# Kernel optimization log

Hardware: AMD Instinct MI355X
Metric: run time of the kernel (lower is better)

Reference implementation:

```python
import jax, jax.numpy as jnp
import numpy as np
import math

B, L, D_IN = 4, 8192, 64
H = 256          # d_model
N2 = 32          # d_state // 2 complex conjugate pairs (S4D)
NL = 4           # n_layers
D_OUT = 10


def setup_inputs() -> dict:
    key = jax.random.key(0)
    ks = jax.random.split(key, 16)
    x = jax.random.normal(ks[0], (B, L, D_IN), dtype=jnp.float32)
    # encoder Linear(d_input, d_model)
    enc_W = jax.random.normal(ks[1], (H, D_IN), dtype=jnp.float32) / np.sqrt(D_IN)
    enc_b = jnp.zeros((H,), dtype=jnp.float32)
    # per-layer S4D parameters (stacked over n_layers)
    log_dt = jax.random.uniform(ks[2], (NL, H), dtype=jnp.float32,
                                minval=math.log(1e-3), maxval=math.log(1e-1))
    log_A_re = jnp.full((NL, H, N2), math.log(0.5), dtype=jnp.float32)
    A_im = jnp.tile(math.pi * jnp.arange(N2, dtype=jnp.float32), (NL, H, 1))
    C_re = jax.random.normal(ks[3], (NL, H, N2), dtype=jnp.float32) * (0.5 ** 0.5)
    C_im = jax.random.normal(ks[4], (NL, H, N2), dtype=jnp.float32) * (0.5 ** 0.5)
    D = jax.random.normal(ks[5], (NL, H), dtype=jnp.float32)
    # S4 block output linear (H -> 2H) followed by GLU
    Wo = jax.random.normal(ks[6], (NL, 2 * H, H), dtype=jnp.float32) / np.sqrt(H)
    bo = jnp.zeros((NL, 2 * H), dtype=jnp.float32)
    # post-norm LayerNorm over d_model
    ln_w = jnp.ones((NL, H), dtype=jnp.float32)
    ln_b = jnp.zeros((NL, H), dtype=jnp.float32)
    # final decoder Linear(d_model, d_output)
    out_W = jax.random.normal(ks[7], (D_OUT, H), dtype=jnp.float32) / np.sqrt(H)
    out_b = jnp.zeros((D_OUT,), dtype=jnp.float32)
    return dict(x=x, enc_W=enc_W, enc_b=enc_b, log_dt=log_dt, log_A_re=log_A_re,
                A_im=A_im, C_re=C_re, C_im=C_im, D=D, Wo=Wo, bo=bo,
                ln_w=ln_w, ln_b=ln_b, out_W=out_W, out_b=out_b)


def _s4d_kernel(log_dt, log_A_re, A_im, C_re, C_im, L):
    # S4D-ZOH-ish (S4D-Lin) kernel: K[h,l] = 2 Re sum_n C~[h,n] exp(l*dt*A[h,n])
    dt = jnp.exp(log_dt)[:, None]                      # (H,1)
    A = -jnp.exp(log_A_re) + 1j * A_im                 # (H,N2)
    dtA = dt * A                                       # (H,N2)
    Ct = (C_re + 1j * C_im) * (jnp.exp(dtA) - 1.0) / A # (H,N2)
    t = jnp.arange(L, dtype=jnp.float32)
    V = jnp.exp(dtA[:, :, None] * t)                   # (H,N2,L) Vandermonde
    return 2.0 * jnp.einsum('hn,hnl->hl', Ct, V).real  # (H,L)


def reference(x, enc_W, enc_b, log_dt, log_A_re, A_im, C_re, C_im, D, Wo, bo,
              ln_w, ln_b, out_W, out_b):
    Bc, Lc, _ = x.shape
    h = x @ enc_W.T + enc_b          # (B,L,H)
    h = h.transpose(0, 2, 1)         # (B,H,L) (transposed layout)
    n_layers = log_dt.shape[0]
    for i in range(n_layers):
        K = _s4d_kernel(log_dt[i], log_A_re[i], A_im[i], C_re[i], C_im[i], Lc)
        # FFT convolution (causal, non-circular via 2L padding)
        Kf = jnp.fft.rfft(K, n=2 * Lc)                       # (H, L+1)
        hf = jnp.fft.rfft(h, n=2 * Lc)                       # (B,H,L+1)
        y = jnp.fft.irfft(hf * Kf, n=2 * Lc)[..., :Lc]
        y = y + D[i][:, None] * h                            # skip D*u
        y = jax.nn.gelu(y)
        # output linear (H -> 2H) + GLU, pointwise over length
        u = jnp.einsum('oh,bhl->bol', Wo[i], y) + bo[i][:, None]
        Hd = h.shape[1]
        z = u[:, :Hd] * jax.nn.sigmoid(u[:, Hd:])
        h = z + h                                            # residual
        # post-norm LayerNorm over channel (d_model) dim
        mu = h.mean(axis=1, keepdims=True)
        var = h.var(axis=1, keepdims=True)
        h = (h - mu) / jnp.sqrt(var + 1e-5) * ln_w[i][:, None] + ln_b[i][:, None]
    h = h.transpose(0, 2, 1)          # (B,L,H)
    return h @ out_W.T + out_b        # (B,L,d_output)
```

## Files before the change

### kernel.cpp

```cpp
#include <hip/hip_runtime.h>
#include <hip/hip_bf16.h>


constexpr int B_ = 4, L_ = 8192, DIN = 64, H_ = 256, N2_ = 32, NL_ = 4, DOUT = 10;
constexpr int LC = 64, CHK = L_ / LC;
constexpr int GCH = B_ * CHK;
constexpr int M_ = B_ * L_;

constexpr size_t OFF_XB   = 0;
constexpr size_t OFF_EWB  = 1048576;
constexpr size_t OFF_WOB  = 8388608;
constexpr size_t OFF_PW   = 8650752;
constexpr size_t OFF_PCT  = 8716288;
constexpr size_t OFF_PWLC = 8781824;
constexpr size_t OFF_PZ   = 8847360;
constexpr size_t OFF_UCM  = 8929280;
constexpr size_t OFF_YCM  = 13123584;
constexpr size_t OFF_MTA  = 17317888;
constexpr size_t OFF_MWA  = 19415040;
constexpr size_t OFF_MVA  = 21512192;

typedef short bf16x8 __attribute__((ext_vector_type(8)));
typedef short short8 __attribute__((ext_vector_type(8)));
typedef float f32x4  __attribute__((ext_vector_type(4)));
typedef int   int2v  __attribute__((ext_vector_type(2)));

__device__ __forceinline__ float b2f(short s) {
    union { float f; unsigned u; } c;
    c.u = ((unsigned)(unsigned short)s) << 16;
    return c.f;
}

__global__ __launch_bounds__(256) void k_params(
    const float* __restrict__ log_dt, const float* __restrict__ log_A_re,
    const float* __restrict__ A_im, const float* __restrict__ C_re,
    const float* __restrict__ C_im, float* __restrict__ ws)
{
    int idx = blockIdx.x * 256 + threadIdx.x;
    if (idx >= NL_ * H_ * N2_) return;
    int i  = idx / (H_ * N2_);
    int hh = (idx / N2_) % H_;
    float dt  = expf(log_dt[i * H_ + hh]);
    float Are = -expf(log_A_re[idx]);
    float Aim = A_im[idx];
    float zre = dt * Are, zim = dt * Aim;
    float er  = expf(zre);
    float wre = er * cosf(zim), wim = er * sinf(zim);
    float d   = Are * Are + Aim * Aim;
    float nre = wre - 1.f, nim = wim;
    float qre = (nre * Are + nim * Aim) / d;
    float qim = (nim * Are - nre * Aim) / d;
    float cr = C_re[idx], ci = C_im[idx];
    float ctre = cr * qre - ci * qim;
    float ctim = cr * qim + ci * qre;
    float er2 = expf(zre * (float)LC);
    float wlre = er2 * cosf(zim * (float)LC);
    float wlim = er2 * sinf(zim * (float)LC);
    ((float2*)(ws + OFF_PW))[idx]   = make_float2(wre, wim);
    ((float2*)(ws + OFF_PCT))[idx]  = make_float2(2.f * ctre, 2.f * ctim);
    ((float2*)(ws + OFF_PWLC))[idx] = make_float2(wlre, wlim);
    ((float2*)(ws + OFF_PZ))[idx]   = make_float2(zre, zim);
}

__global__ __launch_bounds__(256) void k_mats_all(const float* __restrict__ ws,
    __hip_bfloat16* __restrict__ mt, __hip_bfloat16* __restrict__ mw,
    __hip_bfloat16* __restrict__ mv)
{
    int bid = blockIdx.x;
    int layer = bid >> 8, h = bid & 255;
    int lh = layer * H_ + h;
    int tid = threadIdx.x;
    __shared__ float zre[32], zim[32], ctr[32], cti[32], kv[64];
    if (tid < 32) {
        float2 z = ((const float2*)(ws + OFF_PZ))[(size_t)lh * N2_ + tid];
        float2 c = ((const float2*)(ws + OFF_PCT))[(size_t)lh * N2_ + tid];
        zre[tid] = z.x; zim[tid] = z.y; ctr[tid] = c.x; cti[tid] = c.y;
    }
    __syncthreads();
    if (tid < 64) {
        float d = (float)tid, acc = 0.f;
        for (int n = 0; n < 32; n++) {
            float er = expf(zre[n] * d);
            float co = cosf(zim[n] * d), si = sinf(zim[n] * d);
            acc += er * (ctr[n] * co - cti[n] * si);
        }
        kv[tid] = acc;
    }
    __syncthreads();
    {
        int t = tid >> 2, j0 = (tid & 3) * 16;
        alignas(16) __hip_bfloat16 row[16];
        #pragma unroll
        for (int jj = 0; jj < 16; jj++) {
            int j = j0 + jj;
            row[jj] = __float2bfloat16(j <= t ? kv[t - j] : 0.f);
        }
        *(short8*)(mt + (size_t)lh*4096 + t*64 + j0)     = *(short8*)&row[0];
        *(short8*)(mt + (size_t)lh*4096 + t*64 + j0 + 8) = *(short8*)&row[8];
    }
    {
        int n = tid >> 3, j0 = (tid & 7) * 8;
        alignas(16) __hip_bfloat16 rre[8], rim[8];
        #pragma unroll
        for (int jj = 0; jj < 8; jj++) {
            float e = (float)(63 - (j0 + jj));
            float er = expf(zre[n] * e);
            rre[jj] = __float2bfloat16(er * cosf(zim[n] * e));
            rim[jj] = __float2bfloat16(er * sinf(zim[n] * e));
        }
        *(short8*)(mw + (size_t)lh*4096 + (2*n)*64 + j0)   = *(short8*)&rre[0];
        *(short8*)(mw + (size_t)lh*4096 + (2*n+1)*64 + j0) = *(short8*)&rim[0];
    }
    {
        int t = tid >> 2, n0 = (tid & 3) * 8;
        float e = (float)(t + 1);
        alignas(16) __hip_bfloat16 row[16];
        #pragma unroll
        for (int k = 0; k < 8; k++) {
            int n = n0 + k;
            float er = expf(zre[n] * e);
            float wr = er * cosf(zim[n] * e), wi = er * sinf(zim[n] * e);
            row[2*k]   = __float2bfloat16(ctr[n]*wr - cti[n]*wi);
            row[2*k+1] = __float2bfloat16(-(ctr[n]*wi + cti[n]*wr));
        }
        *(short8*)(mv + (size_t)lh*4096 + t*64 + 2*n0)     = *(short8*)&row[0];
        *(short8*)(mv + (size_t)lh*4096 + t*64 + 2*n0 + 8) = *(short8*)&row[8];
    }
}

__global__ __launch_bounds__(256) void k_wcvt(const float* __restrict__ src,
    __hip_bfloat16* __restrict__ dst, int n4)
{
    int i = blockIdx.x * 256 + threadIdx.x;
    if (i >= n4) return;
    float4 v = ((const float4*)src)[i];
    union { __hip_bfloat16 b[4]; uint2 u; } o;
    o.b[0] = __float2bfloat16(v.x); o.b[1] = __float2bfloat16(v.y);
    o.b[2] = __float2bfloat16(v.z); o.b[3] = __float2bfloat16(v.w);
    ((uint2*)dst)[i] = o.u;
}

__global__ __launch_bounds__(256) void k_encoder(const __hip_bfloat16* __restrict__ xb,
    const __hip_bfloat16* __restrict__ ewb, const float* __restrict__ enc_b,
    __hip_bfloat16* __restrict__ u)
{
    __shared__ short lt[256 * 66];
    int tid = threadIdx.x;
    int w = tid >> 6, l = tid & 63, l15 = l & 15, l4 = l >> 4;
    int m0 = blockIdx.x * 64;
    int nv = w * 64;
    f32x4 acc[4][4];
    #pragma unroll
    for (int mi = 0; mi < 4; mi++)
        #pragma unroll
        for (int nj = 0; nj < 4; nj++) acc[mi][nj] = (f32x4)0.f;
    #pragma unroll
    for (int ks = 0; ks < 2; ks++) {
        int k0 = ks * 32 + l4 * 8;
        bf16x8 a[4];
        #pragma unroll
        for (int mi = 0; mi < 4; mi++)
            a[mi] = *(const bf16x8*)(xb + (size_t)(m0 + mi * 16 + l15) * 64 + k0);
        #pragma unroll
        for (int nj = 0; nj < 4; nj++) {
            bf16x8 b = *(const bf16x8*)(ewb + (size_t)(nv + nj * 16 + l15) * 64 + k0);
            #pragma unroll
            for (int mi = 0; mi < 4; mi++)
                acc[mi][nj] = __builtin_amdgcn_mfma_f32_16x16x32_bf16(a[mi], b, acc[mi][nj], 0, 0, 0);
        }
    }
    float bov[4];
    #pragma unroll
    for (int nj = 0; nj < 4; nj++) bov[nj] = enc_b[nv + nj * 16 + l15];
    #pragma unroll
    for (int mi = 0; mi < 4; mi++)
        #pragma unroll
        for (int r = 0; r < 4; r++) {
            int lr = mi * 16 + l4 * 4 + r;
            #pragma unroll
            for (int nj = 0; nj < 4; nj++) {
                int cn = nv + nj * 16 + l15;
                __hip_bfloat16 bv = __float2bfloat16(acc[mi][nj][r] + bov[nj]);
                lt[cn * 66 + lr] = *(short*)&bv;
            }
        }
    __syncthreads();
    #pragma unroll
    for (int q = 0; q < 8; q++)
        *(short8*)(u + (size_t)tid * M_ + m0 + q * 8) = *(short8*)&lt[tid * 66 + q * 8];
}

__global__ __launch_bounds__(256) void k_ssm(const __hip_bfloat16* __restrict__ ucm,
    const __hip_bfloat16* __restrict__ mt, const __hip_bfloat16* __restrict__ mw,
    const __hip_bfloat16* __restrict__ mv, const float* __restrict__ ws, int layer,
    const float* __restrict__ Dp, __hip_bfloat16* __restrict__ ycm)
{
    __shared__ __hip_bfloat16 ulds[L_];
    __shared__ __hip_bfloat16 st[CHK * 64];
    __shared__ float segT[8][32][2];
    int h = blockIdx.x >> 2, b = blockIdx.x & 3;
    int tid = threadIdx.x, w = tid >> 6, l = tid & 63, l15 = l & 15, l4 = l >> 4;
    const __hip_bfloat16* ub = ucm + (size_t)h * M_ + (size_t)b * L_;
    #pragma unroll
    for (int it = 0; it < 4; it++) {
        int e0 = it * 2048 + tid * 8;
        short8 v = *(const short8*)(ub + e0);
        int c = e0 >> 6, e = e0 & 63;
        *(short8*)&ulds[c * 64 + (e ^ ((c & 7) << 3))] = v;
    }
    __syncthreads();
    {
        const __hip_bfloat16* bbase = mw + (size_t)h * 4096 + l15 * 64 + l4 * 8;
        #pragma unroll
        for (int half = 0; half < 2; half++) {
            int g0 = (w + half * 4) * 16;
            int ca = g0 + l15;
            f32x4 acc[4];
            #pragma unroll
            for (int nj = 0; nj < 4; nj++) acc[nj] = (f32x4)0.f;
            #pragma unroll
            for (int ks = 0; ks < 2; ks++) {
                int e = l4 * 8 + ks * 32;
                bf16x8 a = *(const bf16x8*)&ulds[ca * 64 + (e ^ ((ca & 7) << 3))];
                #pragma unroll
                for (int nj = 0; nj < 4; nj++) {
                    bf16x8 bb = *(const bf16x8*)(bbase + nj * 16 * 64 + ks * 32);
                    acc[nj] = __builtin_amdgcn_mfma_f32_16x16x32_bf16(a, bb, acc[nj], 0, 0, 0);
                }
            }
            #pragma unroll
            for (int nj = 0; nj < 4; nj++)
                #pragma unroll
                for (int r = 0; r < 4; r++) {
                    int c = g0 + l4 * 4 + r, e = nj * 16 + l15;
                    st[c * 64 + (e ^ ((c & 7) << 3))] = __float2bfloat16(acc[nj][r]);
                }
        }
    }
    __syncthreads();
    {
        int s = tid >> 5, n = tid & 31;
        float2 wl = ((const float2*)(ws + OFF_PWLC))[(size_t)layer * H_ * N2_ + h * 32 + n];
        float tr = 0.f, ti = 0.f;
        for (int j = 0; j < 16; j++) {
            int c = s * 16 + j;
            __hip_bfloat162* p = (__hip_bfloat162*)&st[c * 64 + ((2 * n) ^ ((c & 7) << 3))];
            float2 v = __bfloat1622float2(*p);
            float nr = fmaf(wl.x, tr, v.x); nr = fmaf(-wl.y, ti, nr);
            float ni = fmaf(wl.x, ti, v.y); ni = fmaf(wl.y, tr, ni);
            tr = nr; ti = ni;
        }
        segT[s][n][0] = tr; segT[s][n][1] = ti;
        __syncthreads();
        float wr = wl.x, wi = wl.y;
        #pragma unroll
        for (int q = 0; q < 4; q++) {
            float nr = wr * wr - wi * wi, ni = 2.f * wr * wi;
            wr = nr; wi = ni;
        }
        float ar = 0.f, ai = 0.f;
        for (int t = 0; t < s; t++) {
            float Tx = segT[t][n][0], Ty = segT[t][n][1];
            float nr = fmaf(wr, ar, Tx); nr = fmaf(-wi, ai, nr);
            float ni = fmaf(wr, ai, Ty); ni = fmaf(wi, ar, ni);
            ar = nr; ai = ni;
        }
        for (int j = 0; j < 16; j++) {
            int c = s * 16 + j;
            __hip_bfloat162* p = (__hip_bfloat162*)&st[c * 64 + ((2 * n) ^ ((c & 7) << 3))];
            float2 v = __bfloat1622float2(*p);
            *p = __float22bfloat162_rn(make_float2(ar, ai));
            float nr = fmaf(wl.x, ar, v.x); nr = fmaf(-wl.y, ai, nr);
            float ni = fmaf(wl.x, ai, v.y); ni = fmaf(wl.y, ar, ni);
            ar = nr; ai = ni;
        }
    }
    __syncthreads();
    {
        const __hip_bfloat16* bt = mt + (size_t)h * 4096 + l15 * 64 + l4 * 8;
        const __hip_bfloat16* bv = mv + (size_t)h * 4096 + l15 * 64 + l4 * 8;
        float Dh = Dp[layer * H_ + h];
        __hip_bfloat16* yb = ycm + (size_t)h * M_ + (size_t)b * L_;
        #pragma unroll
        for (int half = 0; half < 2; half++) {
            int g0 = (w + half * 4) * 16;
            int ca = g0 + l15;
            f32x4 acc[4];
            #pragma unroll
            for (int nj = 0; nj < 4; nj++) acc[nj] = (f32x4)0.f;
            #pragma unroll
            for (int ks = 0; ks < 2; ks++) {
                int e = l4 * 8 + ks * 32;
                bf16x8 a = *(const bf16x8*)&ulds[ca * 64 + (e ^ ((ca & 7) << 3))];
                #pragma unroll
                for (int nj = 0; nj < 4; nj++) {
                    bf16x8 bb = *(const bf16x8*)(bt + nj * 16 * 64 + ks * 32);
                    acc[nj] = __builtin_amdgcn_mfma_f32_16x16x32_bf16(a, bb, acc[nj], 0, 0, 0);
                }
            }
            #pragma unroll
            for (int ks = 0; ks < 2; ks++) {
                int e = l4 * 8 + ks * 32;
                bf16x8 a = *(const bf16x8*)&st[ca * 64 + (e ^ ((ca & 7) << 3))];
                #pragma unroll
                for (int nj = 0; nj < 4; nj++) {
                    bf16x8 bb = *(const bf16x8*)(bv + nj * 16 * 64 + ks * 32);
                    acc[nj] = __builtin_amdgcn_mfma_f32_16x16x32_bf16(a, bb, acc[nj], 0, 0, 0);
                }
            }
            #pragma unroll
            for (int nj = 0; nj < 4; nj++)
                #pragma unroll
                for (int r = 0; r < 4; r++) {
                    int g = g0 + l4 * 4 + r;
                    int e = nj * 16 + l15;
                    float uv = __bfloat162float(ulds[g * 64 + (e ^ ((g & 7) << 3))]);
                    float v = fmaf(Dh, uv, acc[nj][r]);
                    float gg = 0.7978845608028654f * fmaf(0.044715f * v, v * v, v);
                    float yv = v / (1.f + __expf(-2.f * gg));
                    yb[(size_t)g * 64 + nj * 16 + l15] = __float2bfloat16(yv);
                }
        }
    }
}

__global__ __launch_bounds__(256) void k_glu_mfma(
    const __hip_bfloat16* __restrict__ ycm,
    const __hip_bfloat16* __restrict__ wob,
    const float* __restrict__ bo, const float* __restrict__ lnw,
    const float* __restrict__ lnb,
    __hip_bfloat16* __restrict__ u)
{
    __shared__ int buf[8320];
    __shared__ float red[4][32][2];
    int* bufA = buf;
    int* bufR = buf + 4160;
    int tid = threadIdx.x;
    int w = tid >> 6, l = tid & 63, l15 = l & 15, l4 = l >> 4;
    int mb = blockIdx.x * 64;
    int nv = w * 64;
    int p = tid & 127, ph = tid >> 7;
    const __hip_bfloat16* aB = ycm + (size_t)(2 * p) * M_ + mb + ph * 16;
    const __hip_bfloat16* rB = u + (size_t)(2 * p) * M_ + mb + ph * 16;

    short8 A0[4], R0[4], A1[4], R1[4];
    A0[0] = *(const short8*)(aB);          A0[1] = *(const short8*)(aB + 8);
    A0[2] = *(const short8*)(aB + M_);     A0[3] = *(const short8*)(aB + M_ + 8);
    R0[0] = *(const short8*)(rB);          R0[1] = *(const short8*)(rB + 8);
    R0[2] = *(const short8*)(rB + M_);     R0[3] = *(const short8*)(rB + M_ + 8);
    A1[0] = *(const short8*)(aB + 32);     A1[1] = *(const short8*)(aB + 40);
    A1[2] = *(const short8*)(aB + M_ + 32);A1[3] = *(const short8*)(aB + M_ + 40);

    float bov[4], bog[4], lw[4], lb[4];
    #pragma unroll
    for (int nj = 0; nj < 4; nj++) {
        int cn = nv + nj * 16 + l15;
        bov[nj] = bo[cn]; bog[nj] = bo[256 + cn];
        lw[nj] = lnw[cn]; lb[nj] = lnb[cn];
    }

    {
        int* da = bufA + ph * 16 * 130 + p;
        int* dr = bufR + ph * 16 * 130 + p;
        #pragma unroll
        for (int j = 0; j < 8; j++) {
            da[j * 130]       = ((int)(unsigned short)A0[0][j]) | (((int)(unsigned short)A0[2][j]) << 16);
            da[(8 + j) * 130] = ((int)(unsigned short)A0[1][j]) | (((int)(unsigned short)A0[3][j]) << 16);
            dr[j * 130]       = ((int)(unsigned short)R0[0][j]) | (((int)(unsigned short)R0[2][j]) << 16);
            dr[(8 + j) * 130] = ((int)(unsigned short)R0[1][j]) | (((int)(unsigned short)R0[3][j]) << 16);
        }
    }
    __syncthreads();

    int abase0 = l15 * 130 + l4 * 4;
    #pragma unroll
    for (int tile = 0; tile < 2; tile++) {
        int m0 = mb + tile * 32;
        f32x4 accv[2][4], accg[2][4];
        #pragma unroll
        for (int sub = 0; sub < 2; sub++)
            #pragma unroll
            for (int nj = 0; nj < 4; nj++) { accv[sub][nj] = (f32x4)0.f; accg[sub][nj] = (f32x4)0.f; }

        #pragma unroll 2
        for (int ks = 0; ks < 8; ks++) {
            int k0 = ks * 32 + l4 * 8;
            union { int2v d[2]; bf16x8 v; } a0u, a1u;
            a0u.d[0] = *(const int2v*)&bufA[abase0 + ks * 16];
            a0u.d[1] = *(const int2v*)&bufA[abase0 + ks * 16 + 2];
            a1u.d[0] = *(const int2v*)&bufA[abase0 + 16 * 130 + ks * 16];
            a1u.d[1] = *(const int2v*)&bufA[abase0 + 16 * 130 + ks * 16 + 2];
            bf16x8 a0 = a0u.v;
            bf16x8 a1 = a1u.v;
            #pragma unroll
            for (int nj = 0; nj < 4; nj++) {
                bf16x8 bv = *(const bf16x8*)(wob + (size_t)(nv + nj * 16 + l15) * H_ + k0);
                bf16x8 bg = *(const bf16x8*)(wob + (size_t)(256 + nv + nj * 16 + l15) * H_ + k0);
                accv[0][nj] = __builtin_amdgcn_mfma_f32_16x16x32_bf16(a0, bv, accv[0][nj], 0, 0, 0);
                accg[0][nj] = __builtin_amdgcn_mfma_f32_16x16x32_bf16(a0, bg, accg[0][nj], 0, 0, 0);
                accv[1][nj] = __builtin_amdgcn_mfma_f32_16x16x32_bf16(a1, bv, accv[1][nj], 0, 0, 0);
                accg[1][nj] = __builtin_amdgcn_mfma_f32_16x16x32_bf16(a1, bg, accg[1][nj], 0, 0, 0);
            }
        }

        const short* bufRs = (const short*)bufR;
        #pragma unroll
        for (int sub = 0; sub < 2; sub++) {
            #pragma unroll
            for (int r = 0; r < 4; r++) {
                int lr = sub * 16 + l4 * 4 + r;
                float s = 0.f, ss = 0.f;
                #pragma unroll
                for (int nj = 0; nj < 4; nj++) {
                    int cn = nv + nj * 16 + l15;
                    float uv = accv[sub][nj][r] + bov[nj];
                    float ug = accg[sub][nj][r] + bog[nj];
                    float z = uv / (1.f + __expf(-ug));
                    float v = z + b2f(bufRs[lr * 260 + cn]);
                    accv[sub][nj][r] = v;
                    s += v; ss += v * v;
                }
                #pragma unroll
                for (int off = 1; off < 16; off <<= 1) {
                    s  += __shfl_xor(s, off);
                    ss += __shfl_xor(ss, off);
                }
                if (l15 == 0) { red[w][lr][0] = s; red[w][lr][1] = ss; }
            }
        }
        if (tile == 0) {
            R1[0] = *(const short8*)(rB + 32);      R1[1] = *(const short8*)(rB + 40);
            R1[2] = *(const short8*)(rB + M_ + 32); R1[3] = *(const short8*)(rB + M_ + 40);
        }
        __syncthreads();
        short* lt = (short*)buf;
        #pragma unroll
        for (int sub = 0; sub < 2; sub++) {
            #pragma unroll
            for (int r = 0; r < 4; r++) {
                int lr = sub * 16 + l4 * 4 + r;
                float s  = red[0][lr][0] + red[1][lr][0] + red[2][lr][0] + red[3][lr][0];
                float ss = red[0][lr][1] + red[1][lr][1] + red[2][lr][1] + red[3][lr][1];
                float mu = s * (1.f / 256.f);
                float var = ss * (1.f / 256.f) - mu * mu;
                float rstd = rsqrtf(var + 1e-5f);
                #pragma unroll
                for (int nj = 0; nj < 4; nj++) {
                    int cn = nv + nj * 16 + l15;
                    float val = (accv[sub][nj][r] - mu) * rstd * lw[nj] + lb[nj];
                    __hip_bfloat16 bval = __float2bfloat16(val);
                    lt[cn * 34 + lr] = *(short*)&bval;
                }
            }
        }
        __syncthreads();
        #pragma unroll
        for (int q = 0; q < 4; q++)
            *(short8*)(u + (size_t)tid * M_ + m0 + q * 8)
                = *(short8*)&lt[tid * 34 + q * 8];
        if (tile == 0) {
            __syncthreads();
            int* da = bufA + ph * 16 * 130 + p;
            int* dr = bufR + ph * 16 * 130 + p;
            #pragma unroll
            for (int j = 0; j < 8; j++) {
                da[j * 130]       = ((int)(unsigned short)A1[0][j]) | (((int)(unsigned short)A1[2][j]) << 16);
                da[(8 + j) * 130] = ((int)(unsigned short)A1[1][j]) | (((int)(unsigned short)A1[3][j]) << 16);
                dr[j * 130]       = ((int)(unsigned short)R1[0][j]) | (((int)(unsigned short)R1[2][j]) << 16);
                dr[(8 + j) * 130] = ((int)(unsigned short)R1[1][j]) | (((int)(unsigned short)R1[3][j]) << 16);
            }
            __syncthreads();
        }
    }
}

__global__ __launch_bounds__(256) void k_decoder(const __hip_bfloat16* __restrict__ u,
    const float* __restrict__ out_W, const float* __restrict__ out_b,
    float* __restrict__ out)
{
    __shared__ int ds[64 * 130];
    __shared__ float wl[10][260];
    int m0 = blockIdx.x * 64;
    int tid = threadIdx.x;
    {
        int p = tid & 127, ph = tid >> 7;
        const __hip_bfloat16* s0 = u + (size_t)(2 * p) * M_ + m0 + ph * 32;
        const __hip_bfloat16* s1 = s0 + M_;
        short8 y0[4], y1[4];
        #pragma unroll
        for (int q = 0; q < 4; q++) {
            y0[q] = *(const short8*)(s0 + q * 8);
            y1[q] = *(const short8*)(s1 + q * 8);
        }
        int* dst = ds + (ph * 32) * 130 + p;
        #pragma unroll
        for (int q = 0; q < 4; q++)
            #pragma unroll
            for (int j = 0; j < 8; j++)
                dst[(q * 8 + j) * 130] =
                    ((int)(unsigned short)y0[q][j]) | (((int)(unsigned short)y1[q][j]) << 16);
    }
    for (int q = tid; q < 640; q += 256) {
        int r = q / 64, k4 = q % 64;
        *(float4*)&wl[r][k4 * 4] = ((const float4*)out_W)[q];
    }
    __syncthreads();
    int slot = tid & 15;
    if (slot < DOUT) {
        #pragma unroll
        for (int pass = 0; pass < 4; pass++) {
            int pl = pass * 16 + (tid >> 4);
            const int* row = ds + pl * 130;
            float a0 = 0.f, a1 = 0.f;
            #pragma unroll 8
            for (int d = 0; d < 128; d++) {
                int v = row[d];
                a0 = fmaf(b2f((short)(v & 0xffff)),  wl[slot][2 * d],     a0);
                a1 = fmaf(b2f((short)(v >> 16)),     wl[slot][2 * d + 1], a1);
            }
            out[(size_t)(m0 + pl) * DOUT + slot] = a0 + a1 + out_b[slot];
        }
    }
}

extern "C" void kernel_launch(void* const* d_in, const int* in_sizes, int n_in,
                              void* d_out, int out_size, void* d_ws, size_t ws_size,
                              hipStream_t stream)
{
    (void)in_sizes; (void)n_in; (void)out_size; (void)ws_size;
    const float* x        = (const float*)d_in[0];
    const float* enc_W    = (const float*)d_in[1];
    const float* enc_b    = (const float*)d_in[2];
    const float* log_dt   = (const float*)d_in[3];
    const float* log_A_re = (const float*)d_in[4];
    const float* A_im     = (const float*)d_in[5];
    const float* C_re     = (const float*)d_in[6];
    const float* C_im     = (const float*)d_in[7];
    const float* Dp       = (const float*)d_in[8];
    const float* Wo       = (const float*)d_in[9];
    const float* bo       = (const float*)d_in[10];
    const float* lnw      = (const float*)d_in[11];
    const float* lnb      = (const float*)d_in[12];
    const float* out_W    = (const float*)d_in[13];
    const float* out_b    = (const float*)d_in[14];
    float* ws = (float*)d_ws;
    __hip_bfloat16* xb  = (__hip_bfloat16*)(ws + OFF_XB);
    __hip_bfloat16* ewb = (__hip_bfloat16*)(ws + OFF_EWB);
    __hip_bfloat16* u   = (__hip_bfloat16*)(ws + OFF_UCM);
    __hip_bfloat16* ycm = (__hip_bfloat16*)(ws + OFF_YCM);
    __hip_bfloat16* mtA = (__hip_bfloat16*)(ws + OFF_MTA);
    __hip_bfloat16* mwA = (__hip_bfloat16*)(ws + OFF_MWA);
    __hip_bfloat16* mvA = (__hip_bfloat16*)(ws + OFF_MVA);
    __hip_bfloat16* wob = (__hip_bfloat16*)(ws + OFF_WOB);

    k_params<<<NL_ * H_ * N2_ / 256, 256, 0, stream>>>(log_dt, log_A_re, A_im, C_re, C_im, ws);
    k_wcvt<<<(NL_ * 2 * H_ * H_ / 4 + 255) / 256, 256, 0, stream>>>(Wo, wob, NL_ * 2 * H_ * H_ / 4);
    k_wcvt<<<(M_ * DIN / 4 + 255) / 256, 256, 0, stream>>>(x, xb, M_ * DIN / 4);
    k_wcvt<<<(H_ * DIN / 4 + 255) / 256, 256, 0, stream>>>(enc_W, ewb, H_ * DIN / 4);
    k_mats_all<<<NL_ * H_, 256, 0, stream>>>(ws, mtA, mwA, mvA);
    k_encoder<<<M_ / 64, 256, 0, stream>>>(xb, ewb, enc_b, u);
    for (int i = 0; i < NL_; i++) {
        k_ssm<<<H_ * B_, 256, 0, stream>>>(u,
            mtA + (size_t)i * H_ * 4096, mwA + (size_t)i * H_ * 4096,
            mvA + (size_t)i * H_ * 4096, ws, i, Dp, ycm);
        k_glu_mfma<<<M_ / 64, 256, 0, stream>>>(ycm,
            wob + (size_t)i * 2 * H_ * H_, bo + (size_t)i * 2 * H_,
            lnw + (size_t)i * H_, lnb + (size_t)i * H_, u);
    }
    k_decoder<<<M_ / 64, 256, 0, stream>>>(u, out_W, out_b, (float*)d_out);
}
```

Measured before the change: 366.5 us.

## Fuse param setup, x conversion, and decoder into neighboring kernels

```diff
diff --git a/kernel.cpp b/kernel.cpp
--- a/kernel.cpp
+++ b/kernel.cpp
@@ -4,16 +4,11 @@
 
 constexpr int B_ = 4, L_ = 8192, DIN = 64, H_ = 256, N2_ = 32, NL_ = 4, DOUT = 10;
 constexpr int LC = 64, CHK = L_ / LC;
-constexpr int GCH = B_ * CHK;
 constexpr int M_ = B_ * L_;
 
-constexpr size_t OFF_XB   = 0;
 constexpr size_t OFF_EWB  = 1048576;
 constexpr size_t OFF_WOB  = 8388608;
-constexpr size_t OFF_PW   = 8650752;
-constexpr size_t OFF_PCT  = 8716288;
 constexpr size_t OFF_PWLC = 8781824;
-constexpr size_t OFF_PZ   = 8847360;
 constexpr size_t OFF_UCM  = 8929280;
 constexpr size_t OFF_YCM  = 13123584;
 constexpr size_t OFF_MTA  = 17317888;
@@ -22,6 +17,7 @@
 
 typedef short bf16x8 __attribute__((ext_vector_type(8)));
 typedef short short8 __attribute__((ext_vector_type(8)));
+typedef short short4v __attribute__((ext_vector_type(4)));
 typedef float f32x4  __attribute__((ext_vector_type(4)));
 typedef int   int2v  __attribute__((ext_vector_type(2)));
 
@@ -29,103 +25,6 @@
     union { float f; unsigned u; } c;
     c.u = ((unsigned)(unsigned short)s) << 16;
     return c.f;
-}
-
-__global__ __launch_bounds__(256) void k_params(
-    const float* __restrict__ log_dt, const float* __restrict__ log_A_re,
-    const float* __restrict__ A_im, const float* __restrict__ C_re,
-    const float* __restrict__ C_im, float* __restrict__ ws)
-{
-    int idx = blockIdx.x * 256 + threadIdx.x;
-    if (idx >= NL_ * H_ * N2_) return;
-    int i  = idx / (H_ * N2_);
-    int hh = (idx / N2_) % H_;
-    float dt  = expf(log_dt[i * H_ + hh]);
-    float Are = -expf(log_A_re[idx]);
-    float Aim = A_im[idx];
-    float zre = dt * Are, zim = dt * Aim;
-    float er  = expf(zre);
-    float wre = er * cosf(zim), wim = er * sinf(zim);
-    float d   = Are * Are + Aim * Aim;
-    float nre = wre - 1.f, nim = wim;
-    float qre = (nre * Are + nim * Aim) / d;
-    float qim = (nim * Are - nre * Aim) / d;
-    float cr = C_re[idx], ci = C_im[idx];
-    float ctre = cr * qre - ci * qim;
-    float ctim = cr * qim + ci * qre;
-    float er2 = expf(zre * (float)LC);
-    float wlre = er2 * cosf(zim * (float)LC);
-    float wlim = er2 * sinf(zim * (float)LC);
-    ((float2*)(ws + OFF_PW))[idx]   = make_float2(wre, wim);
-    ((float2*)(ws + OFF_PCT))[idx]  = make_float2(2.f * ctre, 2.f * ctim);
-    ((float2*)(ws + OFF_PWLC))[idx] = make_float2(wlre, wlim);
-    ((float2*)(ws + OFF_PZ))[idx]   = make_float2(zre, zim);
-}
-
-__global__ __launch_bounds__(256) void k_mats_all(const float* __restrict__ ws,
-    __hip_bfloat16* __restrict__ mt, __hip_bfloat16* __restrict__ mw,
-    __hip_bfloat16* __restrict__ mv)
-{
-    int bid = blockIdx.x;
-    int layer = bid >> 8, h = bid & 255;
-    int lh = layer * H_ + h;
-    int tid = threadIdx.x;
-    __shared__ float zre[32], zim[32], ctr[32], cti[32], kv[64];
-    if (tid < 32) {
-        float2 z = ((const float2*)(ws + OFF_PZ))[(size_t)lh * N2_ + tid];
-        float2 c = ((const float2*)(ws + OFF_PCT))[(size_t)lh * N2_ + tid];
-        zre[tid] = z.x; zim[tid] = z.y; ctr[tid] = c.x; cti[tid] = c.y;
-    }
-    __syncthreads();
-    if (tid < 64) {
-        float d = (float)tid, acc = 0.f;
-        for (int n = 0; n < 32; n++) {
-            float er = expf(zre[n] * d);
-            float co = cosf(zim[n] * d), si = sinf(zim[n] * d);
-            acc += er * (ctr[n] * co - cti[n] * si);
-        }
-        kv[tid] = acc;
-    }
-    __syncthreads();
-    {
-        int t = tid >> 2, j0 = (tid & 3) * 16;
-        alignas(16) __hip_bfloat16 row[16];
-        #pragma unroll
-        for (int jj = 0; jj < 16; jj++) {
-            int j = j0 + jj;
-            row[jj] = __float2bfloat16(j <= t ? kv[t - j] : 0.f);
-        }
-        *(short8*)(mt + (size_t)lh*4096 + t*64 + j0)     = *(short8*)&row[0];
-        *(short8*)(mt + (size_t)lh*4096 + t*64 + j0 + 8) = *(short8*)&row[8];
-    }
-    {
-        int n = tid >> 3, j0 = (tid & 7) * 8;
-        alignas(16) __hip_bfloat16 rre[8], rim[8];
-        #pragma unroll
-        for (int jj = 0; jj < 8; jj++) {
-            float e = (float)(63 - (j0 + jj));
-            float er = expf(zre[n] * e);
-            rre[jj] = __float2bfloat16(er * cosf(zim[n] * e));
-            rim[jj] = __float2bfloat16(er * sinf(zim[n] * e));
-        }
-        *(short8*)(mw + (size_t)lh*4096 + (2*n)*64 + j0)   = *(short8*)&rre[0];
-        *(short8*)(mw + (size_t)lh*4096 + (2*n+1)*64 + j0) = *(short8*)&rim[0];
-    }
-    {
-        int t = tid >> 2, n0 = (tid & 3) * 8;
-        float e = (float)(t + 1);
-        alignas(16) __hip_bfloat16 row[16];
-        #pragma unroll
-        for (int k = 0; k < 8; k++) {
-            int n = n0 + k;
-            float er = expf(zre[n] * e);
-            float wr = er * cosf(zim[n] * e), wi = er * sinf(zim[n] * e);
-            row[2*k]   = __float2bfloat16(ctr[n]*wr - cti[n]*wi);
-            row[2*k+1] = __float2bfloat16(-(ctr[n]*wi + cti[n]*wr));
-        }
-        *(short8*)(mv + (size_t)lh*4096 + t*64 + 2*n0)     = *(short8*)&row[0];
-        *(short8*)(mv + (size_t)lh*4096 + t*64 + 2*n0 + 8) = *(short8*)&row[8];
-    }
 }
 
 __global__ __launch_bounds__(256) void k_wcvt(const float* __restrict__ src,
@@ -140,15 +39,114 @@
     ((uint2*)dst)[i] = o.u;
 }
 
-__global__ __launch_bounds__(256) void k_encoder(const __hip_bfloat16* __restrict__ xb,
+__global__ __launch_bounds__(256) void k_mats_all(
+    const float* __restrict__ log_dt, const float* __restrict__ log_A_re,
+    const float* __restrict__ A_im, const float* __restrict__ C_re,
+    const float* __restrict__ C_im, float* __restrict__ ws,
+    __hip_bfloat16* __restrict__ mt, __hip_bfloat16* __restrict__ mw,
+    __hip_bfloat16* __restrict__ mv)
+{
+    int bid = blockIdx.x;
+    int layer = bid >> 8, h = bid & 255;
+    int lh = layer * H_ + h;
+    int tid = threadIdx.x;
+    __shared__ float zre[32], zim[32], ctr[32], cti[32], kv[64];
+    if (tid < 32) {
+        int idx = lh * N2_ + tid;
+        float dt  = expf(log_dt[lh]);
+        float Are = -expf(log_A_re[idx]);
+        float Aim = A_im[idx];
+        float zr = dt * Are, zi = dt * Aim;
+        float er = expf(zr);
+        float wre = er * cosf(zi), wim = er * sinf(zi);
+        float d = Are * Are + Aim * Aim;
+        float nre = wre - 1.f, nim = wim;
+        float qre = (nre * Are + nim * Aim) / d;
+        float qim = (nim * Are - nre * Aim) / d;
+        float cr = C_re[idx], ci = C_im[idx];
+        zre[tid] = zr; zim[tid] = zi;
+        ctr[tid] = 2.f * (cr * qre - ci * qim);
+        cti[tid] = 2.f * (cr * qim + ci * qre);
+        float er2 = expf(zr * (float)LC);
+        ((float2*)(ws + OFF_PWLC))[idx] =
+            make_float2(er2 * cosf(zi * (float)LC), er2 * sinf(zi * (float)LC));
+    }
+    __syncthreads();
+    if (tid < 64) {
+        float d = (float)tid, acc = 0.f;
+        for (int n = 0; n < 32; n++) {
+            float er = expf(zre[n] * d);
+            float co = cosf(zim[n] * d), si = sinf(zim[n] * d);
+            acc += er * (ctr[n] * co - cti[n] * si);
+        }
+        kv[tid] = acc;
+    }
+    __syncthreads();
+    {
+        int t = tid >> 2, j0 = (tid & 3) * 16;
+        alignas(16) __hip_bfloat16 row[16];
+        #pragma unroll
+        for (int jj = 0; jj < 16; jj++) {
+            int j = j0 + jj;
+            row[jj] = __float2bfloat16(j <= t ? kv[t - j] : 0.f);
+        }
+        *(short8*)(mt + (size_t)lh*4096 + t*64 + j0)     = *(short8*)&row[0];
+        *(short8*)(mt + (size_t)lh*4096 + t*64 + j0 + 8) = *(short8*)&row[8];
+    }
+    {
+        int n = tid >> 3, j0 = (tid & 7) * 8;
+        alignas(16) __hip_bfloat16 rre[8], rim[8];
+        #pragma unroll
+        for (int jj = 0; jj < 8; jj++) {
+            float e = (float)(63 - (j0 + jj));
+            float er = expf(zre[n] * e);
+            rre[jj] = __float2bfloat16(er * cosf(zim[n] * e));
+            rim[jj] = __float2bfloat16(er * sinf(zim[n] * e));
+        }
+        *(short8*)(mw + (size_t)lh*4096 + (2*n)*64 + j0)   = *(short8*)&rre[0];
+        *(short8*)(mw + (size_t)lh*4096 + (2*n+1)*64 + j0) = *(short8*)&rim[0];
+    }
+    {
+        int t = tid >> 2, n0 = (tid & 3) * 8;
+        float e = (float)(t + 1);
+        alignas(16) __hip_bfloat16 row[16];
+        #pragma unroll
+        for (int k = 0; k < 8; k++) {
+            int n = n0 + k;
+            float er = expf(zre[n] * e);
+            float wr = er * cosf(zim[n] * e), wi = er * sinf(zim[n] * e);
+            row[2*k]   = __float2bfloat16(ctr[n]*wr - cti[n]*wi);
+            row[2*k+1] = __float2bfloat16(-(ctr[n]*wi + cti[n]*wr));
+        }
+        *(short8*)(mv + (size_t)lh*4096 + t*64 + 2*n0)     = *(short8*)&row[0];
+        *(short8*)(mv + (size_t)lh*4096 + t*64 + 2*n0 + 8) = *(short8*)&row[8];
+    }
+}
+
+__global__ __launch_bounds__(256) void k_encoder(const float* __restrict__ x,
     const __hip_bfloat16* __restrict__ ewb, const float* __restrict__ enc_b,
     __hip_bfloat16* __restrict__ u)
 {
-    __shared__ short lt[256 * 66];
+    __shared__ short sbuf[256 * 66];
+    short* xls = sbuf;
     int tid = threadIdx.x;
     int w = tid >> 6, l = tid & 63, l15 = l & 15, l4 = l >> 4;
     int m0 = blockIdx.x * 64;
     int nv = w * 64;
+    {
+        const float4* x4 = (const float4*)x;
+        #pragma unroll
+        for (int q = 0; q < 4; q++) {
+            int f = tid * 4 + q;
+            float4 v = x4[(size_t)m0 * 16 + f];
+            int e = f * 4, row = e >> 6, col = e & 63;
+            alignas(8) __hip_bfloat16 t4[4] = {
+                __float2bfloat16(v.x), __float2bfloat16(v.y),
+                __float2bfloat16(v.z), __float2bfloat16(v.w) };
+            *(short4v*)&xls[row * 72 + col] = *(short4v*)t4;
+        }
+    }
+    __syncthreads();
     f32x4 acc[4][4];
     #pragma unroll
     for (int mi = 0; mi < 4; mi++)
@@ -160,7 +158,7 @@
         bf16x8 a[4];
         #pragma unroll
         for (int mi = 0; mi < 4; mi++)
-            a[mi] = *(const bf16x8*)(xb + (size_t)(m0 + mi * 16 + l15) * 64 + k0);
+            a[mi] = *(const bf16x8*)&xls[(mi * 16 + l15) * 72 + k0];
         #pragma unroll
         for (int nj = 0; nj < 4; nj++) {
             bf16x8 b = *(const bf16x8*)(ewb + (size_t)(nv + nj * 16 + l15) * 64 + k0);
@@ -172,6 +170,7 @@
     float bov[4];
     #pragma unroll
     for (int nj = 0; nj < 4; nj++) bov[nj] = enc_b[nv + nj * 16 + l15];
+    __syncthreads();
     #pragma unroll
     for (int mi = 0; mi < 4; mi++)
         #pragma unroll
@@ -181,13 +180,13 @@
             for (int nj = 0; nj < 4; nj++) {
                 int cn = nv + nj * 16 + l15;
                 __hip_bfloat16 bv = __float2bfloat16(acc[mi][nj][r] + bov[nj]);
-                lt[cn * 66 + lr] = *(short*)&bv;
+                sbuf[cn * 66 + lr] = *(short*)&bv;
             }
         }
     __syncthreads();
     #pragma unroll
     for (int q = 0; q < 8; q++)
-        *(short8*)(u + (size_t)tid * M_ + m0 + q * 8) = *(short8*)&lt[tid * 66 + q * 8];
+        *(short8*)(u + (size_t)tid * M_ + m0 + q * 8) = *(short8*)&sbuf[tid * 66 + q * 8];
 }
 
 __global__ __launch_bounds__(256) void k_ssm(const __hip_bfloat16* __restrict__ ucm,
@@ -324,203 +323,185 @@
     }
 }
 
+#define GLU_BODY(DECODE)                                                        \
+    __shared__ int buf[8320];                                                   \
+    __shared__ float red[4][32][2];                                             \
+    int* bufA = buf;                                                            \
+    int* bufR = buf + 4160;                                                     \
+    int tid = threadIdx.x;                                                      \
+    int w = tid >> 6, l = tid & 63, l15 = l & 15, l4 = l >> 4;                  \
+    int mb = blockIdx.x * 64;                                                   \
+    int nv = w * 64;                                                            \
+    int p = tid & 127, ph = tid >> 7;                                           \
+    const __hip_bfloat16* aB = ycm + (size_t)(2 * p) * M_ + mb + ph * 16;       \
+    const __hip_bfloat16* rB = u + (size_t)(2 * p) * M_ + mb + ph * 16;         \
+    short8 A0[4], R0[4], A1[4], R1[4];                                          \
+    A0[0] = *(const short8*)(aB);          A0[1] = *(const short8*)(aB + 8);    \
+    A0[2] = *(const short8*)(aB + M_);     A0[3] = *(const short8*)(aB + M_ + 8);\
+    R0[0] = *(const short8*)(rB);          R0[1] = *(const short8*)(rB + 8);    \
+    R0[2] = *(const short8*)(rB + M_);     R0[3] = *(const short8*)(rB + M_ + 8);\
+    A1[0] = *(const short8*)(aB + 32);     A1[1] = *(const short8*)(aB + 40);   \
+    A1[2] = *(const short8*)(aB + M_ + 32);A1[3] = *(const short8*)(aB + M_ + 40);\
+    float bov[4], bog[4], lw[4], lb[4];                                         \
+    _Pragma("unroll")                                                           \
+    for (int nj = 0; nj < 4; nj++) {                                            \
+        int cn = nv + nj * 16 + l15;                                            \
+        bov[nj] = bo[cn]; bog[nj] = bo[256 + cn];                               \
+        lw[nj] = lnw[cn]; lb[nj] = lnb[cn];                                     \
+    }                                                                           \
+    {                                                                           \
+        int* da = bufA + ph * 16 * 130 + p;                                     \
+        int* dr = bufR + ph * 16 * 130 + p;                                     \
+        _Pragma("unroll")                                                       \
+        for (int j = 0; j < 8; j++) {                                           \
+            da[j * 130]       = ((int)(unsigned short)A0[0][j]) | (((int)(unsigned short)A0[2][j]) << 16);\
+            da[(8 + j) * 130] = ((int)(unsigned short)A0[1][j]) | (((int)(unsigned short)A0[3][j]) << 16);\
+            dr[j * 130]       = ((int)(unsigned short)R0[0][j]) | (((int)(unsigned short)R0[2][j]) << 16);\
+            dr[(8 + j) * 130] = ((int)(unsigned short)R0[1][j]) | (((int)(unsigned short)R0[3][j]) << 16);\
+        }                                                                       \
+    }                                                                           \
+    __syncthreads();                                                            \
+    int abase0 = l15 * 130 + l4 * 4;                                            \
+    _Pragma("unroll")                                                           \
+    for (int tile = 0; tile < 2; tile++) {                                      \
+        int m0 = mb + tile * 32;                                                \
+        f32x4 accv[2][4], accg[2][4];                                           \
+        _Pragma("unroll")                                                       \
+        for (int sub = 0; sub < 2; sub++)                                       \
+            _Pragma("unroll")                                                   \
+            for (int nj = 0; nj < 4; nj++) { accv[sub][nj] = (f32x4)0.f; accg[sub][nj] = (f32x4)0.f; }\
+        _Pragma("unroll 2")                                                     \
+        for (int ks = 0; ks < 8; ks++) {                                        \
+            int k0 = ks * 32 + l4 * 8;                                          \
+            union { int2v d[2]; bf16x8 v; } a0u, a1u;                           \
+            a0u.d[0] = *(const int2v*)&bufA[abase0 + ks * 16];                  \
+            a0u.d[1] = *(const int2v*)&bufA[abase0 + ks * 16 + 2];              \
+            a1u.d[0] = *(const int2v*)&bufA[abase0 + 16 * 130 + ks * 16];       \
+            a1u.d[1] = *(const int2v*)&bufA[abase0 + 16 * 130 + ks * 16 + 2];   \
+            bf16x8 a0 = a0u.v;                                                  \
+            bf16x8 a1 = a1u.v;                                                  \
+            _Pragma("unroll")                                                   \
+            for (int nj = 0; nj < 4; nj++) {                                    \
+                bf16x8 bv = *(const bf16x8*)(wob + (size_t)(nv + nj * 16 + l15) * H_ + k0);\
+                bf16x8 bg = *(const bf16x8*)(wob + (size_t)(256 + nv + nj * 16 + l15) * H_ + k0);\
+                accv[0][nj] = __builtin_amdgcn_mfma_f32_16x16x32_bf16(a0, bv, accv[0][nj], 0, 0, 0);\
+                accg[0][nj] = __builtin_amdgcn_mfma_f32_16x16x32_bf16(a0, bg, accg[0][nj], 0, 0, 0);\
+                accv[1][nj] = __builtin_amdgcn_mfma_f32_16x16x32_bf16(a1, bv, accv[1][nj], 0, 0, 0);\
+                accg[1][nj] = __builtin_amdgcn_mfma_f32_16x16x32_bf16(a1, bg, accg[1][nj], 0, 0, 0);\
+            }                                                                   \
+        }                                                                       \
+        const short* bufRs = (const short*)bufR;                                \
+        _Pragma("unroll")                                                       \
+        for (int sub = 0; sub < 2; sub++) {                                     \
+            _Pragma("unroll")                                                   \
+            for (int r = 0; r < 4; r++) {                                       \
+                int lr = sub * 16 + l4 * 4 + r;                                 \
+                float s = 0.f, ss = 0.f;                                        \
+                _Pragma("unroll")                                               \
+                for (int nj = 0; nj < 4; nj++) {                                \
+                    int cn = nv + nj * 16 + l15;                                \
+                    float uv = accv[sub][nj][r] + bov[nj];                      \
+                    float ug = accg[sub][nj][r] + bog[nj];                      \
+                    float z = uv / (1.f + __expf(-ug));                         \
+                    float v = z + b2f(bufRs[lr * 260 + cn]);                    \
+                    accv[sub][nj][r] = v;                                       \
+                    s += v; ss += v * v;                                        \
+                }                                                               \
+                _Pragma("unroll")                                               \
+                for (int off = 1; off < 16; off <<= 1) {                        \
+                    s  += __shfl_xor(s, off);                                   \
+                    ss += __shfl_xor(ss, off);                                  \
+                }                                                               \
+                if (l15 == 0) { red[w][lr][0] = s; red[w][lr][1] = ss; }        \
+            }                                                                   \
+        }                                                                       \
+        if (tile == 0) {                                                        \
+            R1[0] = *(const short8*)(rB + 32);      R1[1] = *(const short8*)(rB + 40);\
+            R1[2] = *(const short8*)(rB + M_ + 32); R1[3] = *(const short8*)(rB + M_ + 40);\
+        }                                                                       \
+        __syncthreads();                                                        \
+        short* lt = (short*)buf;                                                \
+        _Pragma("unroll")                                                       \
+        for (int sub = 0; sub < 2; sub++) {                                     \
+            _Pragma("unroll")                                                   \
+            for (int r = 0; r < 4; r++) {                                       \
+                int lr = sub * 16 + l4 * 4 + r;                                 \
+                float s  = red[0][lr][0] + red[1][lr][0] + red[2][lr][0] + red[3][lr][0];\
+                float ss = red[0][lr][1] + red[1][lr][1] + red[2][lr][1] + red[3][lr][1];\
+                float mu = s * (1.f / 256.f);                                   \
+                float var = ss * (1.f / 256.f) - mu * mu;                       \
+                float rstd = rsqrtf(var + 1e-5f);                               \
+                _Pragma("unroll")                                               \
+                for (int nj = 0; nj < 4; nj++) {                                \
+                    int cn = nv + nj * 16 + l15;                                \
+                    float val = (accv[sub][nj][r] - mu) * rstd * lw[nj] + lb[nj];\
+                    __hip_bfloat16 bval = __float2bfloat16(val);                \
+                    lt[cn * 34 + lr] = *(short*)&bval;                          \
+                }                                                               \
+            }                                                                   \
+        }                                                                       \
+        __syncthreads();                                                        \
+        _Pragma("unroll")                                                       \
+        for (int q = 0; q < 4; q++)                                             \
+            *(short8*)(u + (size_t)tid * M_ + m0 + q * 8)                       \
+                = *(short8*)&lt[tid * 34 + q * 8];                              \
+        if (DECODE) {                                                           \
+            float* wl2 = (float*)(buf + 4608);                                  \
+            for (int q = tid; q < 2560; q += 256) {                             \
+                int row = q >> 8, col = q & 255;                                \
+                wl2[row * 257 + col] = out_W[q];                                \
+            }                                                                   \
+            __syncthreads();                                                    \
+            int slot = tid & 15, pbase = tid >> 4;                              \
+            if (slot < DOUT) {                                                  \
+                _Pragma("unroll")                                               \
+                for (int pass = 0; pass < 2; pass++) {                          \
+                    int lr = pass * 16 + pbase;                                 \
+                    const short* ltp = lt + lr;                                 \
+                    const float* wp = wl2 + slot * 257;                         \
+                    float a0 = 0.f, a1 = 0.f;                                   \
+                    _Pragma("unroll 8")                                         \
+                    for (int cn = 0; cn < 256; cn += 2) {                       \
+                        a0 = fmaf(b2f(ltp[cn * 34]),       wp[cn],     a0);     \
+                        a1 = fmaf(b2f(ltp[(cn + 1) * 34]), wp[cn + 1], a1);     \
+                    }                                                           \
+                    out[(size_t)(m0 + lr) * DOUT + slot] = a0 + a1 + out_b[slot];\
+                }                                                               \
+            }                                                                   \
+        }                                                                       \
+        if (tile == 0) {                                                        \
+            __syncthreads();                                                    \
+            int* da = bufA + ph * 16 * 130 + p;                                 \
+            int* dr = bufR + ph * 16 * 130 + p;                                 \
+            _Pragma("unroll")                                                   \
+            for (int j = 0; j < 8; j++) {                                       \
+                da[j * 130]       = ((int)(unsigned short)A1[0][j]) | (((int)(unsigned short)A1[2][j]) << 16);\
+                da[(8 + j) * 130] = ((int)(unsigned short)A1[1][j]) | (((int)(unsigned short)A1[3][j]) << 16);\
+                dr[j * 130]       = ((int)(unsigned short)R1[0][j]) | (((int)(unsigned short)R1[2][j]) << 16);\
+                dr[(8 + j) * 130] = ((int)(unsigned short)R1[1][j]) | (((int)(unsigned short)R1[3][j]) << 16);\
+            }                                                                   \
+            __syncthreads();                                                    \
+        }                                                                       \
+    }
+
 __global__ __launch_bounds__(256) void k_glu_mfma(
-    const __hip_bfloat16* __restrict__ ycm,
-    const __hip_bfloat16* __restrict__ wob,
+    const __hip_bfloat16* __restrict__ ycm, const __hip_bfloat16* __restrict__ wob,
     const float* __restrict__ bo, const float* __restrict__ lnw,
-    const float* __restrict__ lnb,
-    __hip_bfloat16* __restrict__ u)
-{
-    __shared__ int buf[8320];
-    __shared__ float red[4][32][2];
-    int* bufA = buf;
-    int* bufR = buf + 4160;
-    int tid = threadIdx.x;
-    int w = tid >> 6, l = tid & 63, l15 = l & 15, l4 = l >> 4;
-    int mb = blockIdx.x * 64;
-    int nv = w * 64;
-    int p = tid & 127, ph = tid >> 7;
-    const __hip_bfloat16* aB = ycm + (size_t)(2 * p) * M_ + mb + ph * 16;
-    const __hip_bfloat16* rB = u + (size_t)(2 * p) * M_ + mb + ph * 16;
-
-    short8 A0[4], R0[4], A1[4], R1[4];
-    A0[0] = *(const short8*)(aB);          A0[1] = *(const short8*)(aB + 8);
-    A0[2] = *(const short8*)(aB + M_);     A0[3] = *(const short8*)(aB + M_ + 8);
-    R0[0] = *(const short8*)(rB);          R0[1] = *(const short8*)(rB + 8);
-    R0[2] = *(const short8*)(rB + M_);     R0[3] = *(const short8*)(rB + M_ + 8);
-    A1[0] = *(const short8*)(aB + 32);     A1[1] = *(const short8*)(aB + 40);
-    A1[2] = *(const short8*)(aB + M_ + 32);A1[3] = *(const short8*)(aB + M_ + 40);
-
-    float bov[4], bog[4], lw[4], lb[4];
-    #pragma unroll
-    for (int nj = 0; nj < 4; nj++) {
-        int cn = nv + nj * 16 + l15;
-        bov[nj] = bo[cn]; bog[nj] = bo[256 + cn];
-        lw[nj] = lnw[cn]; lb[nj] = lnb[cn];
-    }
-
-    {
-        int* da = bufA + ph * 16 * 130 + p;
-        int* dr = bufR + ph * 16 * 130 + p;
-        #pragma unroll
-        for (int j = 0; j < 8; j++) {
-            da[j * 130]       = ((int)(unsigned short)A0[0][j]) | (((int)(unsigned short)A0[2][j]) << 16);
-            da[(8 + j) * 130] = ((int)(unsigned short)A0[1][j]) | (((int)(unsigned short)A0[3][j]) << 16);
-            dr[j * 130]       = ((int)(unsigned short)R0[0][j]) | (((int)(unsigned short)R0[2][j]) << 16);
-            dr[(8 + j) * 130] = ((int)(unsigned short)R0[1][j]) | (((int)(unsigned short)R0[3][j]) << 16);
-        }
-    }
-    __syncthreads();
-
-    int abase0 = l15 * 130 + l4 * 4;
-    #pragma unroll
-    for (int tile = 0; tile < 2; tile++) {
-        int m0 = mb + tile * 32;
-        f32x4 accv[2][4], accg[2][4];
-        #pragma unroll
-        for (int sub = 0; sub < 2; sub++)
-            #pragma unroll
-            for (int nj = 0; nj < 4; nj++) { accv[sub][nj] = (f32x4)0.f; accg[sub][nj] = (f32x4)0.f; }
-
-        #pragma unroll 2
-        for (int ks = 0; ks < 8; ks++) {
-            int k0 = ks * 32 + l4 * 8;
-            union { int2v d[2]; bf16x8 v; } a0u, a1u;
-            a0u.d[0] = *(const int2v*)&bufA[abase0 + ks * 16];
-            a0u.d[1] = *(const int2v*)&bufA[abase0 + ks * 16 + 2];
-            a1u.d[0] = *(const int2v*)&bufA[abase0 + 16 * 130 + ks * 16];
-            a1u.d[1] = *(const int2v*)&bufA[abase0 + 16 * 130 + ks * 16 + 2];
-            bf16x8 a0 = a0u.v;
-            bf16x8 a1 = a1u.v;
-            #pragma unroll
-            for (int nj = 0; nj < 4; nj++) {
-                bf16x8 bv = *(const bf16x8*)(wob + (size_t)(nv + nj * 16 + l15) * H_ + k0);
-                bf16x8 bg = *(const bf16x8*)(wob + (size_t)(256 + nv + nj * 16 + l15) * H_ + k0);
-                accv[0][nj] = __builtin_amdgcn_mfma_f32_16x16x32_bf16(a0, bv, accv[0][nj], 0, 0, 0);
-                accg[0][nj] = __builtin_amdgcn_mfma_f32_16x16x32_bf16(a0, bg, accg[0][nj], 0, 0, 0);
-                accv[1][nj] = __builtin_amdgcn_mfma_f32_16x16x32_bf16(a1, bv, accv[1][nj], 0, 0, 0);
-                accg[1][nj] = __builtin_amdgcn_mfma_f32_16x16x32_bf16(a1, bg, accg[1][nj], 0, 0, 0);
-            }
-        }
-
-        const short* bufRs = (const short*)bufR;
-        #pragma unroll
-        for (int sub = 0; sub < 2; sub++) {
-            #pragma unroll
-            for (int r = 0; r < 4; r++) {
-                int lr = sub * 16 + l4 * 4 + r;
-                float s = 0.f, ss = 0.f;
-                #pragma unroll
-                for (int nj = 0; nj < 4; nj++) {
-                    int cn = nv + nj * 16 + l15;
-                    float uv = accv[sub][nj][r] + bov[nj];
-                    float ug = accg[sub][nj][r] + bog[nj];
-                    float z = uv / (1.f + __expf(-ug));
-                    float v = z + b2f(bufRs[lr * 260 + cn]);
-                    accv[sub][nj][r] = v;
-                    s += v; ss += v * v;
-                }
-                #pragma unroll
-                for (int off = 1; off < 16; off <<= 1) {
-                    s  += __shfl_xor(s, off);
-                    ss += __shfl_xor(ss, off);
-                }
-                if (l15 == 0) { red[w][lr][0] = s; red[w][lr][1] = ss; }
-            }
-        }
-        if (tile == 0) {
-            R1[0] = *(const short8*)(rB + 32);      R1[1] = *(const short8*)(rB + 40);
-            R1[2] = *(const short8*)(rB + M_ + 32); R1[3] = *(const short8*)(rB + M_ + 40);
-        }
-        __syncthreads();
-        short* lt = (short*)buf;
-        #pragma unroll
-        for (int sub = 0; sub < 2; sub++) {
-            #pragma unroll
-            for (int r = 0; r < 4; r++) {
-                int lr = sub * 16 + l4 * 4 + r;
-                float s  = red[0][lr][0] + red[1][lr][0] + red[2][lr][0] + red[3][lr][0];
-                float ss = red[0][lr][1] + red[1][lr][1] + red[2][lr][1] + red[3][lr][1];
-                float mu = s * (1.f / 256.f);
-                float var = ss * (1.f / 256.f) - mu * mu;
-                float rstd = rsqrtf(var + 1e-5f);
-                #pragma unroll
-                for (int nj = 0; nj < 4; nj++) {
-                    int cn = nv + nj * 16 + l15;
-                    float val = (accv[sub][nj][r] - mu) * rstd * lw[nj] + lb[nj];
-                    __hip_bfloat16 bval = __float2bfloat16(val);
-                    lt[cn * 34 + lr] = *(short*)&bval;
-                }
-            }
-        }
-        __syncthreads();
-        #pragma unroll
-        for (int q = 0; q < 4; q++)
-            *(short8*)(u + (size_t)tid * M_ + m0 + q * 8)
-                = *(short8*)&lt[tid * 34 + q * 8];
-        if (tile == 0) {
-            __syncthreads();
-            int* da = bufA + ph * 16 * 130 + p;
-            int* dr = bufR + ph * 16 * 130 + p;
-            #pragma unroll
-            for (int j = 0; j < 8; j++) {
-                da[j * 130]       = ((int)(unsigned short)A1[0][j]) | (((int)(unsigned short)A1[2][j]) << 16);
-                da[(8 + j) * 130] = ((int)(unsigned short)A1[1][j]) | (((int)(unsigned short)A1[3][j]) << 16);
-                dr[j * 130]       = ((int)(unsigned short)R1[0][j]) | (((int)(unsigned short)R1[2][j]) << 16);
-                dr[(8 + j) * 130] = ((int)(unsigned short)R1[1][j]) | (((int)(unsigned short)R1[3][j]) << 16);
-            }
-            __syncthreads();
-        }
-    }
-}
-
-__global__ __launch_bounds__(256) void k_decoder(const __hip_bfloat16* __restrict__ u,
+    const float* __restrict__ lnb, __hip_bfloat16* __restrict__ u)
+{
+    const float* out_W = nullptr; const float* out_b = nullptr; float* out = nullptr;
+    (void)out_W; (void)out_b; (void)out;
+    GLU_BODY(0)
+}
+
+__global__ __launch_bounds__(256) void k_glu_dec(
+    const __hip_bfloat16* __restrict__ ycm, const __hip_bfloat16* __restrict__ wob,
+    const float* __restrict__ bo, const float* __restrict__ lnw,
+    const float* __restrict__ lnb, __hip_bfloat16* __restrict__ u,
     const float* __restrict__ out_W, const float* __restrict__ out_b,
     float* __restrict__ out)
 {
-    __shared__ int ds[64 * 130];
-    __shared__ float wl[10][260];
-    int m0 = blockIdx.x * 64;
-    int tid = threadIdx.x;
-    {
-        int p = tid & 127, ph = tid >> 7;
-        const __hip_bfloat16* s0 = u + (size_t)(2 * p) * M_ + m0 + ph * 32;
-        const __hip_bfloat16* s1 = s0 + M_;
-        short8 y0[4], y1[4];
-        #pragma unroll
-        for (int q = 0; q < 4; q++) {
-            y0[q] = *(const short8*)(s0 + q * 8);
-            y1[q] = *(const short8*)(s1 + q * 8);
-        }
-        int* dst = ds + (ph * 32) * 130 + p;
-        #pragma unroll
-        for (int q = 0; q < 4; q++)
-            #pragma unroll
-            for (int j = 0; j < 8; j++)
-                dst[(q * 8 + j) * 130] =
-                    ((int)(unsigned short)y0[q][j]) | (((int)(unsigned short)y1[q][j]) << 16);
-    }
-    for (int q = tid; q < 640; q += 256) {
-        int r = q / 64, k4 = q % 64;
-        *(float4*)&wl[r][k4 * 4] = ((const float4*)out_W)[q];
-    }
-    __syncthreads();
-    int slot = tid & 15;
-    if (slot < DOUT) {
-        #pragma unroll
-        for (int pass = 0; pass < 4; pass++) {
-            int pl = pass * 16 + (tid >> 4);
-            const int* row = ds + pl * 130;
-            float a0 = 0.f, a1 = 0.f;
-            #pragma unroll 8
-            for (int d = 0; d < 128; d++) {
-                int v = row[d];
-                a0 = fmaf(b2f((short)(v & 0xffff)),  wl[slot][2 * d],     a0);
-                a1 = fmaf(b2f((short)(v >> 16)),     wl[slot][2 * d + 1], a1);
-            }
-            out[(size_t)(m0 + pl) * DOUT + slot] = a0 + a1 + out_b[slot];
-        }
-    }
+    GLU_BODY(1)
 }
 
 extern "C" void kernel_launch(void* const* d_in, const int* in_sizes, int n_in,
@@ -544,7 +525,6 @@
     const float* out_W    = (const float*)d_in[13];
     const float* out_b    = (const float*)d_in[14];
     float* ws = (float*)d_ws;
-    __hip_bfloat16* xb  = (__hip_bfloat16*)(ws + OFF_XB);
     __hip_bfloat16* ewb = (__hip_bfloat16*)(ws + OFF_EWB);
     __hip_bfloat16* u   = (__hip_bfloat16*)(ws + OFF_UCM);
     __hip_bfloat16* ycm = (__hip_bfloat16*)(ws + OFF_YCM);
@@ -553,19 +533,23 @@
     __hip_bfloat16* mvA = (__hip_bfloat16*)(ws + OFF_MVA);
     __hip_bfloat16* wob = (__hip_bfloat16*)(ws + OFF_WOB);
 
-    k_params<<<NL_ * H_ * N2_ / 256, 256, 0, stream>>>(log_dt, log_A_re, A_im, C_re, C_im, ws);
     k_wcvt<<<(NL_ * 2 * H_ * H_ / 4 + 255) / 256, 256, 0, stream>>>(Wo, wob, NL_ * 2 * H_ * H_ / 4);
-    k_wcvt<<<(M_ * DIN / 4 + 255) / 256, 256, 0, stream>>>(x, xb, M_ * DIN / 4);
     k_wcvt<<<(H_ * DIN / 4 + 255) / 256, 256, 0, stream>>>(enc_W, ewb, H_ * DIN / 4);
-    k_mats_all<<<NL_ * H_, 256, 0, stream>>>(ws, mtA, mwA, mvA);
-    k_encoder<<<M_ / 64, 256, 0, stream>>>(xb, ewb, enc_b, u);
+    k_mats_all<<<NL_ * H_, 256, 0, stream>>>(log_dt, log_A_re, A_im, C_re, C_im,
+                                             ws, mtA, mwA, mvA);
+    k_encoder<<<M_ / 64, 256, 0, stream>>>(x, ewb, enc_b, u);
     for (int i = 0; i < NL_; i++) {
         k_ssm<<<H_ * B_, 256, 0, stream>>>(u,
             mtA + (size_t)i * H_ * 4096, mwA + (size_t)i * H_ * 4096,
             mvA + (size_t)i * H_ * 4096, ws, i, Dp, ycm);
-        k_glu_mfma<<<M_ / 64, 256, 0, stream>>>(ycm,
-            wob + (size_t)i * 2 * H_ * H_, bo + (size_t)i * 2 * H_,
-            lnw + (size_t)i * H_, lnb + (size_t)i * H_, u);
-    }
-    k_decoder<<<M_ / 64, 256, 0, stream>>>(u, out_W, out_b, (float*)d_out);
-}
+        if (i < NL_ - 1)
+            k_glu_mfma<<<M_ / 64, 256, 0, stream>>>(ycm,
+                wob + (size_t)i * 2 * H_ * H_, bo + (size_t)i * 2 * H_,
+                lnw + (size_t)i * H_, lnb + (size_t)i * H_, u);
+        else
+            k_glu_dec<<<M_ / 64, 256, 0, stream>>>(ycm,
+                wob + (size_t)i * 2 * H_ * H_, bo + (size_t)i * 2 * H_,
+                lnw + (size_t)i * H_, lnb + (size_t)i * H_, u,
+                out_W, out_b, (float*)d_out);
+    }
+}
```

Measured after the change: 368.6 us. About the same (+0.6%).
